# Kernel tuning notes

Measured on AMD Instinct MI355X. Metric: run time of the kernel, lower is better.

Reference implementation:

```python
import jax, jax.numpy as jnp
import numpy as np

DIM = 512
NUM_HEADS = 8
HEAD_DIM = DIM // NUM_HEADS
SCALE = HEAD_DIM ** -0.5


def setup_inputs() -> dict:
    key = jax.random.key(0)
    ks = jax.random.split(key, 5)
    B, N = 4, 2048
    x = jax.random.normal(ks[0], (B, N, DIM), dtype=jnp.float32)
    # Learned parameters (torch nn.Linear style: y = x @ W.T + b)
    w_qkv = jax.random.normal(ks[1], (3 * DIM, DIM), dtype=jnp.float32) * (DIM ** -0.5)
    b_qkv = jnp.zeros((3 * DIM,), dtype=jnp.float32)
    w_proj = jax.random.normal(ks[2], (DIM, DIM), dtype=jnp.float32) * (DIM ** -0.5)
    b_proj = jnp.zeros((DIM,), dtype=jnp.float32)
    return {"x": x, "w_qkv": w_qkv, "b_qkv": b_qkv, "w_proj": w_proj, "b_proj": b_proj}


def reference(x, w_qkv, b_qkv, w_proj, b_proj):
    B, N, C = x.shape
    qkv = x @ w_qkv.T + b_qkv                      # [B, N, 3C]
    qkv = qkv.reshape(B, N, 3, NUM_HEADS, HEAD_DIM)
    qkv = jnp.transpose(qkv, (2, 0, 3, 1, 4))      # [3, B, H, N, d]
    q, k, v = qkv[0], qkv[1], qkv[2]
    attn = jnp.einsum("bhqd,bhkd->bhqk", q, k) * SCALE  # [B, H, N, N]
    attn = jax.nn.softmax(attn, axis=-1)
    out = jnp.einsum("bhqk,bhkd->bhqd", attn, v)   # [B, H, N, d]
    out = jnp.transpose(out, (0, 2, 1, 3)).reshape(B, N, C)
    return out @ w_proj.T + b_proj
```

## Files before the change

kernel.cpp:

```cpp
#include <hip/hip_runtime.h>

#define DIM 512
#define NHEAD 8
#define HDIM 64
#define BATCH 4
#define SEQ 2048
#define MTOT (BATCH*SEQ)
#define SCALE 0.125f
#define LOG2E 1.4426950408889634f

typedef __bf16 bf16_t;
typedef __bf16 bf16x8 __attribute__((ext_vector_type(8)));
typedef __bf16 bf16x4 __attribute__((ext_vector_type(4)));
typedef __bf16 bf16x2 __attribute__((ext_vector_type(2)));
typedef float f32x4 __attribute__((ext_vector_type(4)));

#define ASYNC_COPY16(g, l) __builtin_amdgcn_global_load_lds( \
    (const __attribute__((address_space(1))) void*)(g),      \
    (__attribute__((address_space(3))) void*)(l), 16, 0, 0)

#define NX_ELEM  (4194304)
#define NWQ_ELEM (786432)
#define NWP_ELEM (262144)
__global__ __launch_bounds__(256) void cvt_kernel(const float* __restrict__ x,
                                                  const float* __restrict__ wq,
                                                  const float* __restrict__ wp,
                                                  bf16_t* __restrict__ out) {
    int i = (blockIdx.x * 256 + threadIdx.x) * 4;
    const float* src;
    if (i < NX_ELEM)                 src = x  + i;
    else if (i < NX_ELEM + NWQ_ELEM) src = wq + (i - NX_ELEM);
    else                             src = wp + (i - NX_ELEM - NWP_ELEM - NWQ_ELEM + NWP_ELEM);
    float4 v = *reinterpret_cast<const float4*>(src);
    bf16x4 o;
    o[0] = (bf16_t)v.x; o[1] = (bf16_t)v.y; o[2] = (bf16_t)v.z; o[3] = (bf16_t)v.w;
    *reinterpret_cast<bf16x4*>(out + i) = o;
}

__global__ __launch_bounds__(256) void gemm_qkv_kernel(
    const bf16_t* __restrict__ X, const bf16_t* __restrict__ W,
    const float* __restrict__ bias,
    bf16_t* __restrict__ Qo, bf16_t* __restrict__ Ko, bf16_t* __restrict__ Vto)
{
    __shared__ bf16_t smem[16384];
    bf16_t (*As)[64] = reinterpret_cast<bf16_t (*)[64]>(smem);
    bf16_t (*Bs)[64] = reinterpret_cast<bf16_t (*)[64]>(smem + 8192);
    unsigned int* Lw = reinterpret_cast<unsigned int*>(smem);
    const int tid = threadIdx.x;
    const int wave = tid >> 6, lane = tid & 63;
    const int lhi = lane >> 4, llo = lane & 15;
    const int o = blockIdx.x;
    const int x = o & 7, i0 = o >> 3;
    const int m0 = (x * 8 + (i0 & 7)) * 128;
    const int n0 = (i0 >> 3) * 128;
    const int wr = (wave >> 1) * 64, wc = (wave & 1) * 64;
    f32x4 acc[4][4] = {};

    const int srow = wave * 32 + (lane >> 3);
    const int scol = (lane & 7) * 8;
    const bf16_t* gA = X + (size_t)(m0 + srow) * DIM + scol;
    const bf16_t* gB = W + (size_t)(n0 + srow) * DIM + scol;

    for (int k0 = 0; k0 < DIM; k0 += 64) {
        #pragma unroll
        for (int p = 0; p < 4; ++p) {
            ASYNC_COPY16(gA + (size_t)p * 8 * DIM + k0, &As[wave*32 + p*8][0]);
            ASYNC_COPY16(gB + (size_t)p * 8 * DIM + k0, &Bs[wave*32 + p*8][0]);
        }
        __syncthreads();
        #pragma unroll
        for (int ks = 0; ks < 2; ++ks) {
            bf16x8 af[4], bfr[4];
            #pragma unroll
            for (int i = 0; i < 4; ++i)
                af[i] = *reinterpret_cast<const bf16x8*>(&As[wr + i*16 + llo][ks*32 + lhi*8]);
            #pragma unroll
            for (int j = 0; j < 4; ++j)
                bfr[j] = *reinterpret_cast<const bf16x8*>(&Bs[wc + j*16 + llo][ks*32 + lhi*8]);
            __builtin_amdgcn_s_setprio(1);
            #pragma unroll
            for (int i = 0; i < 4; ++i)
                #pragma unroll
                for (int j = 0; j < 4; ++j)
                    acc[i][j] = __builtin_amdgcn_mfma_f32_16x16x32_bf16(af[i], bfr[j], acc[i][j], 0, 0, 0);
            __builtin_amdgcn_s_setprio(0);
        }
        __syncthreads();
    }

    const int b = m0 >> 11, ns0 = m0 & 2047;

    if (n0 < 1024) {
        #pragma unroll
        for (int j = 0; j < 4; ++j) {
            int col = n0 + wc + j*16 + llo;
            int which = col >> 9;
            int hh = (col >> 6) & 7;
            int dd = col & 63;
            float bv = bias[col];
            size_t bh = (size_t)(b * NHEAD + hh);
            #pragma unroll
            for (int i = 0; i < 4; ++i) {
                #pragma unroll
                for (int r = 0; r < 4; ++r) {
                    int ns = ns0 + wr + i*16 + lhi*4 + r;
                    float v = acc[i][j][r] + bv;
                    if (which == 0)
                        Qo[(bh * SEQ + ns) * HDIM + dd] = (bf16_t)(v * (SCALE * LOG2E));
                    else
                        Ko[(bh * SEQ + ns) * HDIM + dd] = (bf16_t)v;
                }
            }
        }
    } else {
        #pragma unroll
        for (int j = 0; j < 4; ++j) {
            int ddc = wc + j*16 + llo;
            float bv = bias[n0 + ddc];
            int xsw = (ddc & 7) * 4;
            #pragma unroll
            for (int i = 0; i < 4; ++i) {
                int dwb = (wr >> 1) + i*8 + lhi*2;
                #pragma unroll
                for (int r2 = 0; r2 < 2; ++r2) {
                    bf16x2 t;
                    t[0] = (bf16_t)(acc[i][j][2*r2]     + bv);
                    t[1] = (bf16_t)(acc[i][j][2*r2 + 1] + bv);
                    Lw[ddc * 64 + ((dwb + r2) ^ xsw)] = __builtin_bit_cast(unsigned int, t);
                }
            }
        }
        __syncthreads();
        const int hh_base = (n0 - 1024) >> 6;
        const int chunk = tid & 15;
        #pragma unroll
        for (int rd = 0; rd < 8; ++rd) {
            int ddc = rd * 16 + (tid >> 4);
            uint4 val = *reinterpret_cast<const uint4*>(
                &Lw[ddc * 64 + ((chunk * 4) ^ ((ddc & 7) * 4))]);
            int dd = ddc & 63;
            int hh = hh_base + (ddc >> 6);
            size_t bh = (size_t)(b * NHEAD + hh);
            *reinterpret_cast<uint4*>(Vto + (bh * HDIM + dd) * SEQ + ns0 + chunk * 8) = val;
        }
    }
}

__global__ __launch_bounds__(512) void attn_kernel(
    const bf16_t* __restrict__ Q, const bf16_t* __restrict__ K,
    const bf16_t* __restrict__ Vt, bf16_t* __restrict__ O)
{
    __shared__ bf16_t Ks[2][64][64];
    __shared__ bf16_t Vs[2][64][64];
    const int tid = threadIdx.x;
    const int wave = tid >> 6, lane = tid & 63;
    const int lhi = lane >> 4, llo = lane & 15;
    const int o = blockIdx.x;
    const int w = (o & 7) * 32 + (o >> 3);
    const int qt = w & 7, bh = w >> 3;
    const bf16_t* Qb = Q + (size_t)bh * SEQ * HDIM;
    const bf16_t* Kb = K + (size_t)bh * SEQ * HDIM;
    const bf16_t* Vb = Vt + (size_t)bh * HDIM * SEQ;
    const int q0 = qt * 256 + wave * 32;

    const int ksr = tid >> 3, kg = tid & 7;
    const int kcol = (kg * 8) ^ ((ksr & 7) * 8);
    const int vd = tid >> 3, vg = tid & 7;
    const int pkA = (32*(vg>>2) + 8*((2*vg)&3)   + 4*((vg>>1)&1)) ^ ((vd & 7) * 8);
    const int pkB = (32*(vg>>2) + 8*((2*vg+1)&3) + 4*((vg>>1)&1)) ^ ((vd & 7) * 8);

    bf16x8 aq[2][2];
    #pragma unroll
    for (int qb = 0; qb < 2; ++qb)
        #pragma unroll
        for (int ks = 0; ks < 2; ++ks)
            aq[qb][ks] = *reinterpret_cast<const bf16x8*>(
                Qb + (size_t)(q0 + qb*16 + llo) * HDIM + ks*32 + lhi*8);

    f32x4 acc_o[2][4] = {};
    float mstat[2], lstat[2];
    lstat[0] = lstat[1] = 0.f;
    const float THR = 8.0f * LOG2E;
    const int NT = SEQ / 64;

    uint4 kreg, vreg;
    bf16x8 apA[2][2], apB[2][2];
    bf16x8 bvA[2][4], bvB[2][4];

    kreg = *reinterpret_cast<const uint4*>(Kb + (size_t)ksr * HDIM + kg*8);
    vreg = *reinterpret_cast<const uint4*>(Vb + (size_t)vd * SEQ + vg*8);
    *reinterpret_cast<uint4*>(&Ks[0][ksr][kcol]) = kreg;
    *reinterpret_cast<uint2*>(&Vs[0][vd][pkA]) = make_uint2(vreg.x, vreg.y);
    *reinterpret_cast<uint2*>(&Vs[0][vd][pkB]) = make_uint2(vreg.z, vreg.w);
    __syncthreads();

    kreg = *reinterpret_cast<const uint4*>(Kb + (size_t)(64 + ksr) * HDIM + kg*8);
    vreg = *reinterpret_cast<const uint4*>(Vb + (size_t)vd * SEQ + 64 + vg*8);

    {
        f32x4 s[2][4] = {};
        __builtin_amdgcn_s_setprio(1);
        #pragma unroll
        for (int kb = 0; kb < 4; ++kb)
            #pragma unroll
            for (int ks = 0; ks < 2; ++ks) {
                bf16x8 kf = *reinterpret_cast<const bf16x8*>(
                    &Ks[0][kb*16 + llo][(ks*32 + lhi*8) ^ ((llo & 7) * 8)]);
                #pragma unroll
                for (int qb = 0; qb < 2; ++qb)
                    s[qb][kb] = __builtin_amdgcn_mfma_f32_16x16x32_bf16(kf, aq[qb][ks], s[qb][kb], 0, 0, 0);
            }
        __builtin_amdgcn_s_setprio(0);
        #pragma unroll
        for (int qb = 0; qb < 2; ++qb) {
            float mx = s[qb][0][0];
            #pragma unroll
            for (int kb = 0; kb < 4; ++kb)
                #pragma unroll
                for (int r = 0; r < 4; ++r) mx = fmaxf(mx, s[qb][kb][r]);
            mx = fmaxf(mx, __shfl_xor(mx, 16, 64));
            mx = fmaxf(mx, __shfl_xor(mx, 32, 64));
            mstat[qb] = mx;
            float rs = 0.f;
            #pragma unroll
            for (int kp = 0; kp < 2; ++kp)
                #pragma unroll
                for (int j = 0; j < 4; ++j) {
                    float p0 = __builtin_amdgcn_exp2f(s[qb][2*kp][j]     - mx);
                    float p1 = __builtin_amdgcn_exp2f(s[qb][2*kp + 1][j] - mx);
                    rs += p0 + p1;
                    apA[qb][kp][j]     = (bf16_t)p0;
                    apA[qb][kp][4 + j] = (bf16_t)p1;
                }
            lstat[qb] = rs;
        }
        #pragma unroll
        for (int kp = 0; kp < 2; ++kp)
            #pragma unroll
            for (int db = 0; db < 4; ++db)
                bvA[kp][db] = *reinterpret_cast<const bf16x8*>(
                    &Vs[0][db*16 + llo][(kp*32 + lhi*8) ^ ((llo & 7) * 8)]);
        *reinterpret_cast<uint4*>(&Ks[1][ksr][kcol]) = kreg;
        *reinterpret_cast<uint2*>(&Vs[1][vd][pkA]) = make_uint2(vreg.x, vreg.y);
        *reinterpret_cast<uint2*>(&Vs[1][vd][pkB]) = make_uint2(vreg.z, vreg.w);
        __syncthreads();
    }

    auto body = [&](int kt, bf16x8 (&apIn)[2][2], bf16x8 (&bvIn)[2][4],
                    bf16x8 (&apOut)[2][2], bf16x8 (&bvOut)[2][4]) {
        const int cur = kt & 1, nxt = cur ^ 1;
        if (kt + 1 < NT) {
            const size_t koff = (size_t)(kt + 1) * 64;
            kreg = *reinterpret_cast<const uint4*>(Kb + (koff + ksr) * HDIM + kg*8);
            vreg = *reinterpret_cast<const uint4*>(Vb + (size_t)vd * SEQ + koff + vg*8);
        }
        f32x4 s[2][4] = {};
        __builtin_amdgcn_s_setprio(1);
        #pragma unroll
        for (int kb = 0; kb < 4; ++kb)
            #pragma unroll
            for (int ks = 0; ks < 2; ++ks) {
                bf16x8 kf = *reinterpret_cast<const bf16x8*>(
                    &Ks[cur][kb*16 + llo][(ks*32 + lhi*8) ^ ((llo & 7) * 8)]);
                #pragma unroll
                for (int qb = 0; qb < 2; ++qb)
                    s[qb][kb] = __builtin_amdgcn_mfma_f32_16x16x32_bf16(kf, aq[qb][ks], s[qb][kb], 0, 0, 0);
            }
        __builtin_amdgcn_s_setprio(0);

        float lmax[2];
        bool ok = true;
        #pragma unroll
        for (int qb = 0; qb < 2; ++qb) {
            float mx = s[qb][0][0];
            #pragma unroll
            for (int kb = 0; kb < 4; ++kb)
                #pragma unroll
                for (int r = 0; r < 4; ++r) mx = fmaxf(mx, s[qb][kb][r]);
            lmax[qb] = mx;
            ok &= (mx <= mstat[qb] + THR);
        }
        if (!__all(ok)) {
            #pragma unroll
            for (int kp = 0; kp < 2; ++kp)
                #pragma unroll
                for (int db = 0; db < 4; ++db)
                    #pragma unroll
                    for (int qb = 0; qb < 2; ++qb)
                        acc_o[qb][db] = __builtin_amdgcn_mfma_f32_16x16x32_bf16(apIn[qb][kp], bvIn[kp][db], acc_o[qb][db], 0, 0, 0);
            #pragma unroll
            for (int kp = 0; kp < 2; ++kp)
                #pragma unroll
                for (int db = 0; db < 4; ++db)
                    #pragma unroll
                    for (int e = 0; e < 8; ++e) bvIn[kp][db][e] = (bf16_t)0.f;
            #pragma unroll
            for (int qb = 0; qb < 2; ++qb) {
                float mx = lmax[qb];
                mx = fmaxf(mx, __shfl_xor(mx, 16, 64));
                mx = fmaxf(mx, __shfl_xor(mx, 32, 64));
                float mold = mstat[qb];
                float mn = fmaxf(mold, mx);
                float alpha = __builtin_amdgcn_exp2f(mold - mn);
                mstat[qb] = mn;
                lstat[qb] *= alpha;
                #pragma unroll
                for (int r = 0; r < 4; ++r) {
                    float av = __shfl(alpha, (lane & 48) >> 2 | r, 64);
                    #pragma unroll
                    for (int db = 0; db < 4; ++db) acc_o[qb][db][r] *= av;
                }
            }
        }

        __builtin_amdgcn_s_setprio(1);
        #pragma unroll
        for (int kp = 0; kp < 2; ++kp) {
            #pragma unroll
            for (int qb = 0; qb < 2; ++qb) {
                float rs = 0.f;
                #pragma unroll
                for (int j = 0; j < 4; ++j) {
                    float p0 = __builtin_amdgcn_exp2f(s[qb][2*kp][j]     - mstat[qb]);
                    float p1 = __builtin_amdgcn_exp2f(s[qb][2*kp + 1][j] - mstat[qb]);
                    rs += p0 + p1;
                    apOut[qb][kp][j]     = (bf16_t)p0;
                    apOut[qb][kp][4 + j] = (bf16_t)p1;
                }
                lstat[qb] += rs;
            }
            #pragma unroll
            for (int db = 0; db < 4; ++db)
                #pragma unroll
                for (int qb = 0; qb < 2; ++qb)
                    acc_o[qb][db] = __builtin_amdgcn_mfma_f32_16x16x32_bf16(apIn[qb][kp], bvIn[kp][db], acc_o[qb][db], 0, 0, 0);
        }
        __builtin_amdgcn_s_setprio(0);

        #pragma unroll
        for (int kp = 0; kp < 2; ++kp)
            #pragma unroll
            for (int db = 0; db < 4; ++db)
                bvOut[kp][db] = *reinterpret_cast<const bf16x8*>(
                    &Vs[cur][db*16 + llo][(kp*32 + lhi*8) ^ ((llo & 7) * 8)]);

        if (kt + 1 < NT) {
            *reinterpret_cast<uint4*>(&Ks[nxt][ksr][kcol]) = kreg;
            *reinterpret_cast<uint2*>(&Vs[nxt][vd][pkA]) = make_uint2(vreg.x, vreg.y);
            *reinterpret_cast<uint2*>(&Vs[nxt][vd][pkB]) = make_uint2(vreg.z, vreg.w);
        }
        __syncthreads();
    };

    for (int tp = 1; tp + 1 < NT; tp += 2) {
        body(tp,     apA, bvA, apB, bvB);
        body(tp + 1, apB, bvB, apA, bvA);
    }
    body(NT - 1, apA, bvA, apB, bvB);

    #pragma unroll
    for (int kp = 0; kp < 2; ++kp)
        #pragma unroll
        for (int db = 0; db < 4; ++db)
            #pragma unroll
            for (int qb = 0; qb < 2; ++qb)
                acc_o[qb][db] = __builtin_amdgcn_mfma_f32_16x16x32_bf16(apB[qb][kp], bvB[kp][db], acc_o[qb][db], 0, 0, 0);

    const int b = bh >> 3, h = bh & 7;
    #pragma unroll
    for (int qb = 0; qb < 2; ++qb) {
        float r = lstat[qb];
        r += __shfl_xor(r, 16, 64);
        r += __shfl_xor(r, 32, 64);
        lstat[qb] = r;
    }
    #pragma unroll
    for (int qb = 0; qb < 2; ++qb) {
        float inv = 1.0f / lstat[qb];
        #pragma unroll
        for (int r = 0; r < 4; ++r) {
            float iv = __shfl(inv, (lane & 48) >> 2 | r, 64);
            int q = q0 + qb*16 + lhi*4 + r;
            #pragma unroll
            for (int db = 0; db < 4; ++db)
                O[(size_t)(b * SEQ + q) * DIM + h*HDIM + db*16 + llo] =
                    (bf16_t)(acc_o[qb][db][r] * iv);
        }
    }
}

__global__ __launch_bounds__(256) void gemm_proj_kernel(
    const bf16_t* __restrict__ X, const bf16_t* __restrict__ W,
    const float* __restrict__ bias, float* __restrict__ out)
{
    __shared__ bf16_t As[128][64];
    __shared__ bf16_t Bs[64][64];
    const int tid = threadIdx.x;
    const int wave = tid >> 6, lane = tid & 63;
    const int lhi = lane >> 4, llo = lane & 15;
    const int o = blockIdx.x;
    const int x = o & 7, i0 = o >> 3;
    const int m0 = (x * 8 + (i0 & 7)) * 128;
    const int n0 = (i0 >> 3) * 64;
    const int wr = (wave >> 1) * 64, wc = (wave & 1) * 32;
    f32x4 acc[4][2] = {};

    const int srow = wave * 32 + (lane >> 3);
    const int srowB = wave * 16 + (lane >> 3);
    const int scol = (lane & 7) * 8;
    const bf16_t* gA = X + (size_t)(m0 + srow) * DIM + scol;
    const bf16_t* gB = W + (size_t)(n0 + srowB) * DIM + scol;

    for (int k0 = 0; k0 < DIM; k0 += 64) {
        #pragma unroll
        for (int p = 0; p < 4; ++p)
            ASYNC_COPY16(gA + (size_t)p * 8 * DIM + k0, &As[wave*32 + p*8][0]);
        #pragma unroll
        for (int p = 0; p < 2; ++p)
            ASYNC_COPY16(gB + (size_t)p * 8 * DIM + k0, &Bs[wave*16 + p*8][0]);
        __syncthreads();
        #pragma unroll
        for (int ks = 0; ks < 2; ++ks) {
            bf16x8 af[4], bfr[2];
            #pragma unroll
            for (int i = 0; i < 4; ++i)
                af[i] = *reinterpret_cast<const bf16x8*>(&As[wr + i*16 + llo][ks*32 + lhi*8]);
            #pragma unroll
            for (int j = 0; j < 2; ++j)
                bfr[j] = *reinterpret_cast<const bf16x8*>(&Bs[wc + j*16 + llo][ks*32 + lhi*8]);
            __builtin_amdgcn_s_setprio(1);
            #pragma unroll
            for (int i = 0; i < 4; ++i)
                #pragma unroll
                for (int j = 0; j < 2; ++j)
                    acc[i][j] = __builtin_amdgcn_mfma_f32_16x16x32_bf16(af[i], bfr[j], acc[i][j], 0, 0, 0);
            __builtin_amdgcn_s_setprio(0);
        }
        __syncthreads();
    }

    #pragma unroll
    for (int j = 0; j < 2; ++j) {
        int col = n0 + wc + j*16 + llo;
        float bv = bias[col];
        #pragma unroll
        for (int i = 0; i < 4; ++i)
            #pragma unroll
            for (int r = 0; r < 4; ++r) {
                int m = m0 + wr + i*16 + lhi*4 + r;
                out[(size_t)m * DIM + col] = acc[i][j][r] + bv;
            }
    }
}

extern "C" void kernel_launch(void* const* d_in, const int* in_sizes, int n_in,
                              void* d_out, int out_size, void* d_ws, size_t ws_size,
                              hipStream_t stream) {
    const float* x      = (const float*)d_in[0];
    const float* w_qkv  = (const float*)d_in[1];
    const float* b_qkv  = (const float*)d_in[2];
    const float* w_proj = (const float*)d_in[3];
    const float* b_proj = (const float*)d_in[4];
    float* out = (float*)d_out;

    const size_t NX  = (size_t)MTOT * DIM;
    const size_t NWQ = (size_t)3 * DIM * DIM;
    const size_t NWP = (size_t)DIM * DIM;
    const size_t NQ  = (size_t)BATCH * NHEAD * SEQ * HDIM;

    bf16_t* Xb    = (bf16_t*)d_ws;
    bf16_t* Wqkv  = Xb + NX;
    bf16_t* Wproj = Wqkv + NWQ;
    bf16_t* Qb    = Wproj + NWP;
    bf16_t* Kb    = Qb + NQ;
    bf16_t* Vtb   = Kb + NQ;
    bf16_t* AOb   = Vtb + NQ;

    cvt_kernel<<<(int)((NX + NWQ + NWP) / 1024), 256, 0, stream>>>(x, w_qkv, w_proj, Xb);

    gemm_qkv_kernel<<<768, 256, 0, stream>>>(Xb, Wqkv, b_qkv, Qb, Kb, Vtb);

    attn_kernel<<<256, 512, 0, stream>>>(Qb, Kb, Vtb, AOb);

    gemm_proj_kernel<<<512, 256, 0, stream>>>(AOb, Wproj, b_proj, out);
}
```

Measured before the change: 90.93 us.

## Widen attention K/V LDS tiles to 128 keys to halve block barriers

Doubles the K and V shared-memory tiles from 64 to 128 keys, and splits each tile into two 64-key substeps that share one prefetch and one __syncthreads. This halves the block-wide barriers and global-load rounds per key sweep, so waves stall less often at synchronisation. In exchange, LDS use doubles and each thread holds two staging register sets, which can reduce occupancy and raise register pressure. The V-pack index and the cvt source-offset expression are also rewritten into simpler forms that compute the same values.

Measured after the change: 116.1 us. 27.7% more time.

```diff
diff --git a/kernel.cpp b/kernel.cpp
--- a/kernel.cpp
+++ b/kernel.cpp
@@ -30,7 +30,7 @@
     const float* src;
     if (i < NX_ELEM)                 src = x  + i;
     else if (i < NX_ELEM + NWQ_ELEM) src = wq + (i - NX_ELEM);
-    else                             src = wp + (i - NX_ELEM - NWP_ELEM - NWQ_ELEM + NWP_ELEM);
+    else                             src = wp + (i - NX_ELEM - NWQ_ELEM);
     float4 v = *reinterpret_cast<const float4*>(src);
     bf16x4 o;
     o[0] = (bf16_t)v.x; o[1] = (bf16_t)v.y; o[2] = (bf16_t)v.z; o[3] = (bf16_t)v.w;
@@ -150,8 +150,8 @@
     const bf16_t* __restrict__ Q, const bf16_t* __restrict__ K,
     const bf16_t* __restrict__ Vt, bf16_t* __restrict__ O)
 {
-    __shared__ bf16_t Ks[2][64][64];
-    __shared__ bf16_t Vs[2][64][64];
+    __shared__ bf16_t Ks[2][128][64];
+    __shared__ bf16_t Vs[2][64][128];
     const int tid = threadIdx.x;
     const int wave = tid >> 6, lane = tid & 63;
     const int lhi = lane >> 4, llo = lane & 15;
@@ -166,8 +166,9 @@
     const int ksr = tid >> 3, kg = tid & 7;
     const int kcol = (kg * 8) ^ ((ksr & 7) * 8);
     const int vd = tid >> 3, vg = tid & 7;
-    const int pkA = (32*(vg>>2) + 8*((2*vg)&3)   + 4*((vg>>1)&1)) ^ ((vd & 7) * 8);
-    const int pkB = (32*(vg>>2) + 8*((2*vg+1)&3) + 4*((vg>>1)&1)) ^ ((vd & 7) * 8);
+    const int sw = (vd & 7) * 8;
+    const int pkApre = 32*(vg>>2) + 16*(vg&1) + 4*((vg>>1)&1);
+    const int pkA = pkApre ^ sw, pkB = (pkApre + 8) ^ sw;
 
     bf16x8 aq[2][2];
     #pragma unroll
@@ -181,21 +182,27 @@
     float mstat[2], lstat[2];
     lstat[0] = lstat[1] = 0.f;
     const float THR = 8.0f * LOG2E;
-    const int NT = SEQ / 64;
-
-    uint4 kreg, vreg;
+
+    uint4 kreg[2], vreg[2];
     bf16x8 apA[2][2], apB[2][2];
     bf16x8 bvA[2][4], bvB[2][4];
 
-    kreg = *reinterpret_cast<const uint4*>(Kb + (size_t)ksr * HDIM + kg*8);
-    vreg = *reinterpret_cast<const uint4*>(Vb + (size_t)vd * SEQ + vg*8);
-    *reinterpret_cast<uint4*>(&Ks[0][ksr][kcol]) = kreg;
-    *reinterpret_cast<uint2*>(&Vs[0][vd][pkA]) = make_uint2(vreg.x, vreg.y);
-    *reinterpret_cast<uint2*>(&Vs[0][vd][pkB]) = make_uint2(vreg.z, vreg.w);
+    kreg[0] = *reinterpret_cast<const uint4*>(Kb + (size_t)ksr * HDIM + kg*8);
+    kreg[1] = *reinterpret_cast<const uint4*>(Kb + (size_t)(ksr + 64) * HDIM + kg*8);
+    vreg[0] = *reinterpret_cast<const uint4*>(Vb + (size_t)vd * SEQ + vg*8);
+    vreg[1] = *reinterpret_cast<const uint4*>(Vb + (size_t)vd * SEQ + 64 + vg*8);
+    *reinterpret_cast<uint4*>(&Ks[0][ksr][kcol]) = kreg[0];
+    *reinterpret_cast<uint4*>(&Ks[0][ksr + 64][kcol]) = kreg[1];
+    *reinterpret_cast<uint2*>(&Vs[0][vd][pkA]) = make_uint2(vreg[0].x, vreg[0].y);
+    *reinterpret_cast<uint2*>(&Vs[0][vd][pkB]) = make_uint2(vreg[0].z, vreg[0].w);
+    *reinterpret_cast<uint2*>(&Vs[0][vd][64 + pkA]) = make_uint2(vreg[1].x, vreg[1].y);
+    *reinterpret_cast<uint2*>(&Vs[0][vd][64 + pkB]) = make_uint2(vreg[1].z, vreg[1].w);
     __syncthreads();
 
-    kreg = *reinterpret_cast<const uint4*>(Kb + (size_t)(64 + ksr) * HDIM + kg*8);
-    vreg = *reinterpret_cast<const uint4*>(Vb + (size_t)vd * SEQ + 64 + vg*8);
+    kreg[0] = *reinterpret_cast<const uint4*>(Kb + (size_t)(128 + ksr) * HDIM + kg*8);
+    kreg[1] = *reinterpret_cast<const uint4*>(Kb + (size_t)(192 + ksr) * HDIM + kg*8);
+    vreg[0] = *reinterpret_cast<const uint4*>(Vb + (size_t)vd * SEQ + 128 + vg*8);
+    vreg[1] = *reinterpret_cast<const uint4*>(Vb + (size_t)vd * SEQ + 192 + vg*8);
 
     {
         f32x4 s[2][4] = {};
@@ -240,31 +247,29 @@
             for (int db = 0; db < 4; ++db)
                 bvA[kp][db] = *reinterpret_cast<const bf16x8*>(
                     &Vs[0][db*16 + llo][(kp*32 + lhi*8) ^ ((llo & 7) * 8)]);
-        *reinterpret_cast<uint4*>(&Ks[1][ksr][kcol]) = kreg;
-        *reinterpret_cast<uint2*>(&Vs[1][vd][pkA]) = make_uint2(vreg.x, vreg.y);
-        *reinterpret_cast<uint2*>(&Vs[1][vd][pkB]) = make_uint2(vreg.z, vreg.w);
-        __syncthreads();
-    }
-
-    auto body = [&](int kt, bf16x8 (&apIn)[2][2], bf16x8 (&bvIn)[2][4],
+    }
+
+    auto body = [&](int s, bf16x8 (&apIn)[2][2], bf16x8 (&bvIn)[2][4],
                     bf16x8 (&apOut)[2][2], bf16x8 (&bvOut)[2][4]) {
-        const int cur = kt & 1, nxt = cur ^ 1;
-        if (kt + 1 < NT) {
-            const size_t koff = (size_t)(kt + 1) * 64;
-            kreg = *reinterpret_cast<const uint4*>(Kb + (koff + ksr) * HDIM + kg*8);
-            vreg = *reinterpret_cast<const uint4*>(Vb + (size_t)vd * SEQ + koff + vg*8);
-        }
-        f32x4 s[2][4] = {};
+        const int tile = s >> 1, half = s & 1, cur = tile & 1, rb = half * 64;
+        if (half == 0 && tile + 1 < 16) {
+            const size_t koff = (size_t)(tile + 1) * 128;
+            kreg[0] = *reinterpret_cast<const uint4*>(Kb + (koff + ksr) * HDIM + kg*8);
+            kreg[1] = *reinterpret_cast<const uint4*>(Kb + (koff + 64 + ksr) * HDIM + kg*8);
+            vreg[0] = *reinterpret_cast<const uint4*>(Vb + (size_t)vd * SEQ + koff + vg*8);
+            vreg[1] = *reinterpret_cast<const uint4*>(Vb + (size_t)vd * SEQ + koff + 64 + vg*8);
+        }
+        f32x4 s2[2][4] = {};
         __builtin_amdgcn_s_setprio(1);
         #pragma unroll
         for (int kb = 0; kb < 4; ++kb)
             #pragma unroll
             for (int ks = 0; ks < 2; ++ks) {
                 bf16x8 kf = *reinterpret_cast<const bf16x8*>(
-                    &Ks[cur][kb*16 + llo][(ks*32 + lhi*8) ^ ((llo & 7) * 8)]);
+                    &Ks[cur][rb + kb*16 + llo][(ks*32 + lhi*8) ^ ((llo & 7) * 8)]);
                 #pragma unroll
                 for (int qb = 0; qb < 2; ++qb)
-                    s[qb][kb] = __builtin_amdgcn_mfma_f32_16x16x32_bf16(kf, aq[qb][ks], s[qb][kb], 0, 0, 0);
+                    s2[qb][kb] = __builtin_amdgcn_mfma_f32_16x16x32_bf16(kf, aq[qb][ks], s2[qb][kb], 0, 0, 0);
             }
         __builtin_amdgcn_s_setprio(0);
 
@@ -272,11 +277,11 @@
         bool ok = true;
         #pragma unroll
         for (int qb = 0; qb < 2; ++qb) {
-            float mx = s[qb][0][0];
+            float mx = s2[qb][0][0];
             #pragma unroll
             for (int kb = 0; kb < 4; ++kb)
                 #pragma unroll
-                for (int r = 0; r < 4; ++r) mx = fmaxf(mx, s[qb][kb][r]);
+                for (int r = 0; r < 4; ++r) mx = fmaxf(mx, s2[qb][kb][r]);
             lmax[qb] = mx;
             ok &= (mx <= mstat[qb] + THR);
         }
@@ -321,8 +326,8 @@
                 float rs = 0.f;
                 #pragma unroll
                 for (int j = 0; j < 4; ++j) {
-                    float p0 = __builtin_amdgcn_exp2f(s[qb][2*kp][j]     - mstat[qb]);
-                    float p1 = __builtin_amdgcn_exp2f(s[qb][2*kp + 1][j] - mstat[qb]);
+                    float p0 = __builtin_amdgcn_exp2f(s2[qb][2*kp][j]     - mstat[qb]);
+                    float p1 = __builtin_amdgcn_exp2f(s2[qb][2*kp + 1][j] - mstat[qb]);
                     rs += p0 + p1;
                     apOut[qb][kp][j]     = (bf16_t)p0;
                     apOut[qb][kp][4 + j] = (bf16_t)p1;
@@ -342,21 +347,25 @@
             #pragma unroll
             for (int db = 0; db < 4; ++db)
                 bvOut[kp][db] = *reinterpret_cast<const bf16x8*>(
-                    &Vs[cur][db*16 + llo][(kp*32 + lhi*8) ^ ((llo & 7) * 8)]);
-
-        if (kt + 1 < NT) {
-            *reinterpret_cast<uint4*>(&Ks[nxt][ksr][kcol]) = kreg;
-            *reinterpret_cast<uint2*>(&Vs[nxt][vd][pkA]) = make_uint2(vreg.x, vreg.y);
-            *reinterpret_cast<uint2*>(&Vs[nxt][vd][pkB]) = make_uint2(vreg.z, vreg.w);
-        }
-        __syncthreads();
+                    &Vs[cur][db*16 + llo][(rb + kp*32 + lhi*8) ^ ((llo & 7) * 8)]);
+
+        if (half == 1 && tile + 1 < 16) {
+            const int nb = cur ^ 1;
+            *reinterpret_cast<uint4*>(&Ks[nb][ksr][kcol]) = kreg[0];
+            *reinterpret_cast<uint4*>(&Ks[nb][ksr + 64][kcol]) = kreg[1];
+            *reinterpret_cast<uint2*>(&Vs[nb][vd][pkA]) = make_uint2(vreg[0].x, vreg[0].y);
+            *reinterpret_cast<uint2*>(&Vs[nb][vd][pkB]) = make_uint2(vreg[0].z, vreg[0].w);
+            *reinterpret_cast<uint2*>(&Vs[nb][vd][64 + pkA]) = make_uint2(vreg[1].x, vreg[1].y);
+            *reinterpret_cast<uint2*>(&Vs[nb][vd][64 + pkB]) = make_uint2(vreg[1].z, vreg[1].w);
+            __syncthreads();
+        }
     };
 
-    for (int tp = 1; tp + 1 < NT; tp += 2) {
-        body(tp,     apA, bvA, apB, bvB);
-        body(tp + 1, apB, bvB, apA, bvA);
-    }
-    body(NT - 1, apA, bvA, apB, bvB);
+    for (int sp = 1; sp + 1 < 32; sp += 2) {
+        body(sp,     apA, bvA, apB, bvB);
+        body(sp + 1, apB, bvB, apA, bvA);
+    }
+    body(31, apA, bvA, apB, bvB);
 
     #pragma unroll
     for (int kp = 0; kp < 2; ++kp)
```
